# Kernel tuning notes

Measured on AMD Instinct MI355X. Metric: run time of the kernel, lower is better.

Reference implementation:

```python
import jax, jax.numpy as jnp
import numpy as np

B, S, TAGSET = 64, 512, 62
T = TAGSET + 2  # + START (index T-2) and END (index T-1)


def setup_inputs() -> dict:
    key = jax.random.key(0)
    k1, k2, k3, k4 = jax.random.split(key, 4)
    feats = jax.random.normal(k1, (B, S, T), dtype=jnp.float32)
    # transitions param (torch init is zeros; small random for a non-degenerate baseline)
    transitions = 0.01 * jax.random.normal(k2, (T, T), dtype=jnp.float32)
    # variable-length contiguous-prefix mask (CRF assumes mask[:, 0] == 1)
    lengths = jax.random.randint(k3, (B,), S // 2, S + 1)
    mask = (jnp.arange(S)[None, :] < lengths[:, None]).astype(jnp.int32)
    tags = jax.random.randint(k4, (B, S), 0, TAGSET).astype(jnp.int32)
    return {"feats": feats, "transitions": transitions, "mask": mask, "tags": tags}


def _nll(feats, transitions, mask, tags):
    b, s, t = feats.shape
    maskb = mask.astype(bool)
    feats_t = jnp.transpose(feats, (1, 0, 2))  # [S, B, T]
    mask_t = jnp.transpose(maskb, (1, 0))       # [S, B]

    # ---- partition function (calculate_PZ) ----
    start = t - 2
    init_part = feats_t[0] + transitions[start][None, :]  # [B, T]

    def step(part, inp):
        f_t, m_t = inp  # f_t: [B, T] emissions, m_t: [B]
        # scores[b, i, j] = part[b, i] + transitions[i, j] + f_t[b, j]
        cur = jax.nn.logsumexp(
            part[:, :, None] + transitions[None, :, :] + f_t[:, None, :], axis=1
        )  # [B, T]
        part = jnp.where(m_t[:, None], cur, part)
        return part, None

    part, _ = jax.lax.scan(step, init_part, (feats_t[1:], mask_t[1:]))
    final = jax.nn.logsumexp(part[:, :, None] + transitions[None, :, :], axis=1)
    forward_score = final[:, t - 1].sum()  # transition into END

    # ---- gold score (score_sentence) ----
    tags = tags.astype(jnp.int32)
    prev = jnp.concatenate(
        [jnp.full((b, 1), start, dtype=jnp.int32), tags[:, :-1]], axis=1
    )  # [B, S] previous tag (START at t=0)
    emit = jnp.take_along_axis(feats, tags[..., None].astype(jnp.int32), axis=2)[..., 0]
    trans = transitions[prev, tags]  # [B, S]
    tg_energy = jnp.where(maskb, emit + trans, 0.0).sum()
    lengths = mask.astype(jnp.int32).sum(axis=1)  # [B]
    end_ids = jnp.take_along_axis(tags, (lengths - 1)[:, None], axis=1)[:, 0]
    end_energy = transitions[end_ids, t - 1].sum()
    gold_score = tg_energy + end_energy

    return forward_score - gold_score


def reference(feats, transitions, mask, tags):
    return _nll(feats, transitions, mask, tags)
```

## Files before the change

kernel.cpp:

```cpp
#include <hip/hip_runtime.h>


#define SS 512
#define TT 64
#define CC 8
#define KCH 64
#define START_TAG 62
#define END_TAG 63
#define LOG2E_F 1.44269504088896340736f
#define LN2_F 0.69314718055994530942f

#define WS_ECOL_OFF 4194304
#define WS_GOLD_OFF 4325376
#define WS_EF_OFF   4325632
#define MSTR 72

typedef float v4f __attribute__((ext_vector_type(4)));
typedef _Float16 h4 __attribute__((ext_vector_type(4)));
typedef __fp16 c2 __attribute__((ext_vector_type(2)));
union H4u { h4 v; struct { c2 lo, hi; } p; };

__global__ __launch_bounds__(256, 1)
void crf_prep(const float* __restrict__ feats, const float* __restrict__ trans,
              const int* __restrict__ mask, const int* __restrict__ tags,
              float* __restrict__ out, float* __restrict__ Gg,
              _Float16* __restrict__ Ef) {
    const int c = blockIdx.x;
    const int tid = threadIdx.x;
    const int w = tid >> 6;
    __shared__ int li[4];
    __shared__ float gf[4];
    __shared__ int Lsh;

    int m = mask[c * SS + tid] + mask[c * SS + 256 + tid];
#pragma unroll
    for (int s_ = 1; s_ < 64; s_ <<= 1) m += __shfl_xor(m, s_, 64);
    if ((tid & 63) == 0) li[w] = m;
    __syncthreads();
    if (tid == 0) Lsh = li[0] + li[1] + li[2] + li[3];
    __syncthreads();
    const int Lc = Lsh;

    float g = 0.f;
#pragma unroll
    for (int rep = 0; rep < 2; ++rep) {
        int t = tid + rep * 256;
        if (t < Lc) {
            int cur = tags[c * SS + t];
            int prev = (t == 0) ? START_TAG : tags[c * SS + t - 1];
            g += feats[(size_t)c * SS * TT + (size_t)t * TT + cur] + trans[prev * TT + cur];
        }
    }
    if (tid == 0) g += trans[tags[c * SS + Lc - 1] * TT + END_TAG];
#pragma unroll
    for (int s_ = 1; s_ < 64; s_ <<= 1) g += __shfl_xor(g, s_, 64);
    if ((tid & 63) == 0) gf[w] = g;
    __syncthreads();
    if (tid == 0) Gg[c] = gf[0] + gf[1] + gf[2] + gf[3];

    if (c == 0) {
#pragma unroll
        for (int k = 0; k < 16; ++k) {
            int idx = tid + k * 256;
            Ef[idx] = (_Float16)expf(trans[idx]);
        }
        if (tid == 0) out[0] = 0.f;
    }
}

__device__ __forceinline__ void cstep(const h4 (&A)[4][4], h4 (&B)[4],
                                      float* __restrict__ emb, float& fq,
                                      const float* __restrict__ fcol, int tload,
                                      int q, int l, int& esum, int& esc) {
    v4f z = {0.f, 0.f, 0.f, 0.f};
    v4f D[4];
#pragma unroll
    for (int mt = 0; mt < 4; ++mt) {
        v4f a = __builtin_amdgcn_mfma_f32_16x16x16f16(A[mt][0], B[0], z, 0, 0, 0);
        a = __builtin_amdgcn_mfma_f32_16x16x16f16(A[mt][1], B[1], a, 0, 0, 0);
        v4f b = __builtin_amdgcn_mfma_f32_16x16x16f16(A[mt][2], B[2], z, 0, 0, 0);
        b = __builtin_amdgcn_mfma_f32_16x16x16f16(A[mt][3], B[3], b, 0, 0, 0);
        D[mt] = a + b;
    }
    v4f em[4];
#pragma unroll
    for (int mt = 0; mt < 4; ++mt) em[mt] = *(const v4f*)(emb + 16 * mt + 4 * q);
    emb[l] = __builtin_amdgcn_exp2f(fq * LOG2E_F);
    fq = fcol[(size_t)tload * TT];
    esum += esc;
    float scf = __uint_as_float((unsigned)(127 - esc) << 23);
    v4f qs[4];
#pragma unroll
    for (int mt = 0; mt < 4; ++mt) qs[mt] = D[mt] * (em[mt] * scf);
#pragma unroll
    for (int mt = 0; mt < 4; ++mt) {
        H4u u;
        u.p.lo = __builtin_amdgcn_cvt_pkrtz(qs[mt].x, qs[mt].y);
        u.p.hi = __builtin_amdgcn_cvt_pkrtz(qs[mt].z, qs[mt].w);
        B[mt] = u.v;
    }
    unsigned u0 = (unsigned)__builtin_amdgcn_readfirstlane((int)__float_as_uint(qs[0].x));
    esc = (int)((u0 >> 23) & 255u) - 127;
}

__global__ __launch_bounds__(256, 1)
void crf_chunks(const float* __restrict__ feats, const int* __restrict__ mask,
                const _Float16* __restrict__ Ef, unsigned short* __restrict__ Pg,
                int* __restrict__ Eg) {
    __shared__ float emA[4][2][TT];
    __shared__ float emB[4][2][TT];
    __shared__ __align__(16) _Float16 mld[TT * MSTR];
    __shared__ int ebuf[4];

    const int blk = blockIdx.x;
    const int chain = blk >> 3, c = blk & 7;
    const int tid = threadIdx.x;
    const int w = tid >> 6, l = tid & 63;
    const int n16 = l & 15, q = l >> 4;
    const int ncol = 16 * w + n16;

    h4 A[4][4];
#pragma unroll
    for (int mt = 0; mt < 4; ++mt)
#pragma unroll
        for (int ks = 0; ks < 4; ++ks) {
            h4 a;
#pragma unroll
            for (int e = 0; e < 4; ++e)
                a[e] = Ef[(16 * ks + 4 * q + e) * TT + 16 * mt + n16];
            A[mt][ks] = a;
        }

    const int* mp = mask + chain * SS;
    int msum = 0;
#pragma unroll
    for (int k = 0; k < 8; ++k) msum += mp[k * 64 + l];
#pragma unroll
    for (int s_ = 1; s_ < 64; s_ <<= 1) msum += __shfl_xor(msum, s_, 64);
    const int L = msum;

    const int t0a = 1 + KCH * c;
    const int t0b = t0a + 32;
    int nliveA = (L - 1) - KCH * c;
    nliveA = nliveA < 0 ? 0 : (nliveA > 32 ? 32 : nliveA);
    int nliveB = (L - 1) - KCH * c - 32;
    nliveB = nliveB < 0 ? 0 : (nliveB > 32 ? 32 : nliveB);

    h4 BA[4], BB[4];
#pragma unroll
    for (int ks = 0; ks < 4; ++ks) {
        h4 b;
#pragma unroll
        for (int j = 0; j < 4; ++j)
            b[j] = (_Float16)((16 * ks + 4 * q + j == ncol) ? 1.f : 0.f);
        BA[ks] = b;
        BB[ks] = b;
    }

    const float* fcol = feats + (size_t)chain * SS * TT + l;
#define CLAMP_T(x) ((x) < SS ? (x) : SS - 1)
    emA[w][0][l] = __builtin_amdgcn_exp2f(fcol[(size_t)CLAMP_T(t0a) * TT] * LOG2E_F);
    emA[w][1][l] = __builtin_amdgcn_exp2f(fcol[(size_t)CLAMP_T(t0a + 1) * TT] * LOG2E_F);
    emB[w][0][l] = __builtin_amdgcn_exp2f(fcol[(size_t)CLAMP_T(t0b) * TT] * LOG2E_F);
    emB[w][1][l] = __builtin_amdgcn_exp2f(fcol[(size_t)CLAMP_T(t0b + 1) * TT] * LOG2E_F);
    float fqA0 = fcol[(size_t)CLAMP_T(t0a + 2) * TT];
    float fqA1 = fcol[(size_t)CLAMP_T(t0a + 3) * TT];
    float fqB0 = fcol[(size_t)CLAMP_T(t0b + 2) * TT];
    float fqB1 = fcol[(size_t)CLAMP_T(t0b + 3) * TT];

    int esumA = 0, escA = 0, esumB = 0, escB = 0;

    const int nB2 = nliveB & ~1;
    int s = 0;
    for (; s < nB2; s += 2) {
        cstep(A, BA, &emA[w][0][0], fqA0, fcol, CLAMP_T(t0a + s + 4), q, l, esumA, escA);
        cstep(A, BB, &emB[w][0][0], fqB0, fcol, CLAMP_T(t0b + s + 4), q, l, esumB, escB);
        cstep(A, BA, &emA[w][1][0], fqA1, fcol, CLAMP_T(t0a + s + 5), q, l, esumA, escA);
        cstep(A, BB, &emB[w][1][0], fqB1, fcol, CLAMP_T(t0b + s + 5), q, l, esumB, escB);
    }
    if (nliveB & 1)
        cstep(A, BB, &emB[w][0][0], fqB0, fcol, SS - 1, q, l, esumB, escB);
    for (; s + 1 < nliveA; s += 2) {
        cstep(A, BA, &emA[w][0][0], fqA0, fcol, CLAMP_T(t0a + s + 4), q, l, esumA, escA);
        cstep(A, BA, &emA[w][1][0], fqA1, fcol, CLAMP_T(t0a + s + 5), q, l, esumA, escA);
    }
    if (s < nliveA)
        cstep(A, BA, &emA[w][0][0], fqA0, fcol, SS - 1, q, l, esumA, escA);
#undef CLAMP_T

    if (l == 0) ebuf[w] = esumB;
    __syncthreads();
    int eBmax = max(max(ebuf[0], ebuf[1]), max(ebuf[2], ebuf[3]));
    {
        _Float16 scl = (_Float16)ldexpf(1.f, esumB - eBmax);
        h4 s4 = {scl, scl, scl, scl};
#pragma unroll
        for (int ks = 0; ks < 4; ++ks) {
            h4 v = BB[ks] * s4;
#pragma unroll
            for (int j = 0; j < 4; ++j)
                mld[(16 * ks + 4 * q + j) * MSTR + ncol] = v[j];
        }
    }
    __syncthreads();
    h4 AH[4][4];
#pragma unroll
    for (int mt = 0; mt < 4; ++mt)
#pragma unroll
        for (int ks = 0; ks < 4; ++ks)
            AH[mt][ks] = *(const h4*)(mld + (16 * mt + n16) * MSTR + 16 * ks + 4 * q);
    v4f z = {0.f, 0.f, 0.f, 0.f};
    h4 Rf[4];
#pragma unroll
    for (int mt = 0; mt < 4; ++mt) {
        v4f a = __builtin_amdgcn_mfma_f32_16x16x16f16(AH[mt][0], BA[0], z, 0, 0, 0);
        a = __builtin_amdgcn_mfma_f32_16x16x16f16(AH[mt][1], BA[1], a, 0, 0, 0);
        v4f b = __builtin_amdgcn_mfma_f32_16x16x16f16(AH[mt][2], BA[2], z, 0, 0, 0);
        b = __builtin_amdgcn_mfma_f32_16x16x16f16(AH[mt][3], BA[3], b, 0, 0, 0);
        v4f d = a + b;
        H4u u;
        u.p.lo = __builtin_amdgcn_cvt_pkrtz(d.x, d.y);
        u.p.hi = __builtin_amdgcn_cvt_pkrtz(d.z, d.w);
        Rf[mt] = u.v;
    }
    __syncthreads();
#pragma unroll
    for (int mt = 0; mt < 4; ++mt)
#pragma unroll
        for (int j = 0; j < 4; ++j)
            mld[(16 * mt + 4 * q + j) * MSTR + ncol] = Rf[mt][j];
    __syncthreads();
    {
        const size_t base = ((size_t)chain * CC + c) * 4096;
        int r = tid >> 2, cb = tid & 3;
        const uint4* src = (const uint4*)(mld + r * MSTR + cb * 16);
        uint4* dst = (uint4*)(Pg + base + r * TT + cb * 16);
        dst[0] = src[0];
        dst[1] = src[1];
    }
    if (q == 0) Eg[(chain * CC + c) * TT + ncol] = esumA + eBmax;
}

__global__ __launch_bounds__(64, 1)
void crf_combine(const float* __restrict__ feats, const float* __restrict__ trans,
                 const unsigned short* __restrict__ Pg, const int* __restrict__ Eg,
                 const float* __restrict__ Gg, float* __restrict__ out) {
    __shared__ __align__(16) float yl[TT];
    const int chain = blockIdx.x;
    const int j = threadIdx.x;

    float part0 = feats[(size_t)chain * SS * TT + j] + trans[START_TAG * TT + j];
    float M0 = part0;
#pragma unroll
    for (int m = 1; m < 64; m <<= 1) M0 = fmaxf(M0, __shfl_xor(M0, m, 64));
    float x = exp2f((part0 - M0) * LOG2E_F);
    int esumX = 0;

    for (int c = 0; c < CC; ++c) {
        int e = Eg[(chain * CC + c) * TT + j];
        int emax = e;
#pragma unroll
        for (int m = 1; m < 64; m <<= 1) emax = max(emax, __shfl_xor(emax, m, 64));
        yl[j] = ldexpf(x, e - emax);
        float yv[64];
        {
            const uint4* yq = (const uint4*)yl;
#pragma unroll
            for (int i = 0; i < 16; ++i) {
                union { uint4 u; float f[4]; } cv;
                cv.u = yq[i];
                yv[4 * i + 0] = cv.f[0]; yv[4 * i + 1] = cv.f[1];
                yv[4 * i + 2] = cv.f[2]; yv[4 * i + 3] = cv.f[3];
            }
        }
        const uint4* rp = (const uint4*)(Pg + ((size_t)chain * CC + c) * 4096 + (size_t)j * TT);
        float acc = 0.f;
#pragma unroll
        for (int i = 0; i < 8; ++i) {
            union { uint4 u; _Float16 h[8]; } pv;
            pv.u = rp[i];
#pragma unroll
            for (int k2 = 0; k2 < 8; ++k2)
                acc = __builtin_fmaf((float)pv.h[k2], yv[8 * i + k2], acc);
        }
        float am = acc;
#pragma unroll
        for (int m = 1; m < 64; m <<= 1) am = fmaxf(am, __shfl_xor(am, m, 64));
        int e0 = (int)((__float_as_uint(am) >> 23) & 255u) - 127;
        x = ldexpf(acc, -e0);
        esumX += e0 + emax;
    }

    float val = x * expf(trans[j * TT + END_TAG]);
#pragma unroll
    for (int m = 1; m < 64; m <<= 1) val += __shfl_xor(val, m, 64);
    float fwd = logf(val) + (float)esumX * LN2_F + M0;
    if (j == 0) atomicAdd(out, fwd);

    if (chain == 0) {
        float gv = Gg[j];
#pragma unroll
        for (int m = 1; m < 64; m <<= 1) gv += __shfl_xor(gv, m, 64);
        if (j == 0) atomicAdd(out, -gv);
    }
}

extern "C" void kernel_launch(void* const* d_in, const int* in_sizes, int n_in,
                              void* d_out, int out_size, void* d_ws, size_t ws_size,
                              hipStream_t stream) {
    const float* feats = (const float*)d_in[0];
    const float* trans = (const float*)d_in[1];
    const int*   mask  = (const int*)d_in[2];
    const int*   tags  = (const int*)d_in[3];
    float* out = (float*)d_out;
    unsigned short* Pg = (unsigned short*)d_ws;
    int*       Eg = (int*)((char*)d_ws + WS_ECOL_OFF);
    float*     Gg = (float*)((char*)d_ws + WS_GOLD_OFF);
    _Float16*  Ef = (_Float16*)((char*)d_ws + WS_EF_OFF);

    crf_prep<<<dim3(64), dim3(256), 0, stream>>>(feats, trans, mask, tags, out, Gg, Ef);
    crf_chunks<<<dim3(64 * CC), dim3(256), 0, stream>>>(feats, mask, Ef, Pg, Eg);
    crf_combine<<<dim3(64), dim3(64), 0, stream>>>(feats, trans, Pg, Eg, Gg, out);
}
```

Measured before the change: 112.1 us.

## Fuse prep into chunk kernel, split chains into more chunks, prefetch in combine

Removes the separate prep kernel by folding the gold-score work into extra blocks of the chunk kernel, and computes exp(transitions) per block instead of reading a precomputed fp16 table. Each chain is split into 16 chunks when the workspace allows, giving more blocks and shorter sequential scans. Chunks now write both half-products separately instead of merging them with an in-block MFMA, so the combine kernel does twice as many sequential matvec steps; it prefetches the next product matrix to hide load latency. This trades shorter chunk critical paths and one fewer launch for a longer serial combine stage.

```diff
diff --git a/kernel.cpp b/kernel.cpp
--- a/kernel.cpp
+++ b/kernel.cpp
@@ -3,70 +3,16 @@
 
 #define SS 512
 #define TT 64
-#define CC 8
-#define KCH 64
 #define START_TAG 62
 #define END_TAG 63
 #define LOG2E_F 1.44269504088896340736f
 #define LN2_F 0.69314718055994530942f
-
-#define WS_ECOL_OFF 4194304
-#define WS_GOLD_OFF 4325376
-#define WS_EF_OFF   4325632
 #define MSTR 72
 
 typedef float v4f __attribute__((ext_vector_type(4)));
 typedef _Float16 h4 __attribute__((ext_vector_type(4)));
 typedef __fp16 c2 __attribute__((ext_vector_type(2)));
 union H4u { h4 v; struct { c2 lo, hi; } p; };
-
-__global__ __launch_bounds__(256, 1)
-void crf_prep(const float* __restrict__ feats, const float* __restrict__ trans,
-              const int* __restrict__ mask, const int* __restrict__ tags,
-              float* __restrict__ out, float* __restrict__ Gg,
-              _Float16* __restrict__ Ef) {
-    const int c = blockIdx.x;
-    const int tid = threadIdx.x;
-    const int w = tid >> 6;
-    __shared__ int li[4];
-    __shared__ float gf[4];
-    __shared__ int Lsh;
-
-    int m = mask[c * SS + tid] + mask[c * SS + 256 + tid];
-#pragma unroll
-    for (int s_ = 1; s_ < 64; s_ <<= 1) m += __shfl_xor(m, s_, 64);
-    if ((tid & 63) == 0) li[w] = m;
-    __syncthreads();
-    if (tid == 0) Lsh = li[0] + li[1] + li[2] + li[3];
-    __syncthreads();
-    const int Lc = Lsh;
-
-    float g = 0.f;
-#pragma unroll
-    for (int rep = 0; rep < 2; ++rep) {
-        int t = tid + rep * 256;
-        if (t < Lc) {
-            int cur = tags[c * SS + t];
-            int prev = (t == 0) ? START_TAG : tags[c * SS + t - 1];
-            g += feats[(size_t)c * SS * TT + (size_t)t * TT + cur] + trans[prev * TT + cur];
-        }
-    }
-    if (tid == 0) g += trans[tags[c * SS + Lc - 1] * TT + END_TAG];
-#pragma unroll
-    for (int s_ = 1; s_ < 64; s_ <<= 1) g += __shfl_xor(g, s_, 64);
-    if ((tid & 63) == 0) gf[w] = g;
-    __syncthreads();
-    if (tid == 0) Gg[c] = gf[0] + gf[1] + gf[2] + gf[3];
-
-    if (c == 0) {
-#pragma unroll
-        for (int k = 0; k < 16; ++k) {
-            int idx = tid + k * 256;
-            Ef[idx] = (_Float16)expf(trans[idx]);
-        }
-        if (tid == 0) out[0] = 0.f;
-    }
-}
 
 __device__ __forceinline__ void cstep(const h4 (&A)[4][4], h4 (&B)[4],
                                       float* __restrict__ emb, float& fq,
@@ -103,18 +49,60 @@
     esc = (int)((u0 >> 23) & 255u) - 127;
 }
 
+template <int CCT>
 __global__ __launch_bounds__(256, 1)
-void crf_chunks(const float* __restrict__ feats, const int* __restrict__ mask,
-                const _Float16* __restrict__ Ef, unsigned short* __restrict__ Pg,
-                int* __restrict__ Eg) {
-    __shared__ float emA[4][2][TT];
-    __shared__ float emB[4][2][TT];
+void crf_chunks(const float* __restrict__ feats, const float* __restrict__ trans,
+                const int* __restrict__ mask, const int* __restrict__ tags,
+                float* __restrict__ out, unsigned short* __restrict__ Pg,
+                int* __restrict__ Eg, float* __restrict__ Gg) {
+    constexpr int KCH_T = SS / CCT;
+    constexpr int HALF = KCH_T / 2;
+    constexpr int M = 2 * CCT;
+
+    __shared__ __align__(16) float emA[4][2][TT];
+    __shared__ __align__(16) float emB[4][2][TT];
     __shared__ __align__(16) _Float16 mld[TT * MSTR];
-    __shared__ int ebuf[4];
+    __shared__ int li[4];
+    __shared__ float gf[4];
+    __shared__ int Lsh;
 
     const int blk = blockIdx.x;
-    const int chain = blk >> 3, c = blk & 7;
     const int tid = threadIdx.x;
+
+    if (blk >= 64 * CCT) {
+        const int chain = blk - 64 * CCT;
+        const int w = tid >> 6;
+        int m = mask[chain * SS + tid] + mask[chain * SS + 256 + tid];
+#pragma unroll
+        for (int s_ = 1; s_ < 64; s_ <<= 1) m += __shfl_xor(m, s_, 64);
+        if ((tid & 63) == 0) li[w] = m;
+        __syncthreads();
+        if (tid == 0) Lsh = li[0] + li[1] + li[2] + li[3];
+        __syncthreads();
+        const int Lc = Lsh;
+
+        float g = 0.f;
+#pragma unroll
+        for (int rep = 0; rep < 2; ++rep) {
+            int t = tid + rep * 256;
+            if (t < Lc) {
+                int cur = tags[chain * SS + t];
+                int prev = (t == 0) ? START_TAG : tags[chain * SS + t - 1];
+                g += feats[(size_t)chain * SS * TT + (size_t)t * TT + cur]
+                   + trans[prev * TT + cur];
+            }
+        }
+        if (tid == 0) g += trans[tags[chain * SS + Lc - 1] * TT + END_TAG];
+#pragma unroll
+        for (int s_ = 1; s_ < 64; s_ <<= 1) g += __shfl_xor(g, s_, 64);
+        if ((tid & 63) == 0) gf[w] = g;
+        __syncthreads();
+        if (tid == 0) Gg[chain] = gf[0] + gf[1] + gf[2] + gf[3];
+        if (chain == 0 && tid == 0) out[0] = 0.f;
+        return;
+    }
+
+    const int chain = blk / CCT, c = blk % CCT;
     const int w = tid >> 6, l = tid & 63;
     const int n16 = l & 15, q = l >> 4;
     const int ncol = 16 * w + n16;
@@ -127,7 +115,7 @@
             h4 a;
 #pragma unroll
             for (int e = 0; e < 4; ++e)
-                a[e] = Ef[(16 * ks + 4 * q + e) * TT + 16 * mt + n16];
+                a[e] = (_Float16)expf(trans[(16 * ks + 4 * q + e) * TT + 16 * mt + n16]);
             A[mt][ks] = a;
         }
 
@@ -139,12 +127,12 @@
     for (int s_ = 1; s_ < 64; s_ <<= 1) msum += __shfl_xor(msum, s_, 64);
     const int L = msum;
 
-    const int t0a = 1 + KCH * c;
-    const int t0b = t0a + 32;
-    int nliveA = (L - 1) - KCH * c;
-    nliveA = nliveA < 0 ? 0 : (nliveA > 32 ? 32 : nliveA);
-    int nliveB = (L - 1) - KCH * c - 32;
-    nliveB = nliveB < 0 ? 0 : (nliveB > 32 ? 32 : nliveB);
+    const int t0a = 1 + KCH_T * c;
+    const int t0b = t0a + HALF;
+    int nliveA = (L - 1) - KCH_T * c;
+    nliveA = nliveA < 0 ? 0 : (nliveA > HALF ? HALF : nliveA);
+    int nliveB = (L - 1) - KCH_T * c - HALF;
+    nliveB = nliveB < 0 ? 0 : (nliveB > HALF ? HALF : nliveB);
 
     h4 BA[4], BB[4];
 #pragma unroll
@@ -188,63 +176,44 @@
         cstep(A, BA, &emA[w][0][0], fqA0, fcol, SS - 1, q, l, esumA, escA);
 #undef CLAMP_T
 
-    if (l == 0) ebuf[w] = esumB;
-    __syncthreads();
-    int eBmax = max(max(ebuf[0], ebuf[1]), max(ebuf[2], ebuf[3]));
-    {
-        _Float16 scl = (_Float16)ldexpf(1.f, esumB - eBmax);
-        h4 s4 = {scl, scl, scl, scl};
-#pragma unroll
-        for (int ks = 0; ks < 4; ++ks) {
-            h4 v = BB[ks] * s4;
-#pragma unroll
-            for (int j = 0; j < 4; ++j)
-                mld[(16 * ks + 4 * q + j) * MSTR + ncol] = v[j];
-        }
-    }
-    __syncthreads();
-    h4 AH[4][4];
-#pragma unroll
-    for (int mt = 0; mt < 4; ++mt)
-#pragma unroll
-        for (int ks = 0; ks < 4; ++ks)
-            AH[mt][ks] = *(const h4*)(mld + (16 * mt + n16) * MSTR + 16 * ks + 4 * q);
-    v4f z = {0.f, 0.f, 0.f, 0.f};
-    h4 Rf[4];
-#pragma unroll
-    for (int mt = 0; mt < 4; ++mt) {
-        v4f a = __builtin_amdgcn_mfma_f32_16x16x16f16(AH[mt][0], BA[0], z, 0, 0, 0);
-        a = __builtin_amdgcn_mfma_f32_16x16x16f16(AH[mt][1], BA[1], a, 0, 0, 0);
-        v4f b = __builtin_amdgcn_mfma_f32_16x16x16f16(AH[mt][2], BA[2], z, 0, 0, 0);
-        b = __builtin_amdgcn_mfma_f32_16x16x16f16(AH[mt][3], BA[3], b, 0, 0, 0);
-        v4f d = a + b;
-        H4u u;
-        u.p.lo = __builtin_amdgcn_cvt_pkrtz(d.x, d.y);
-        u.p.hi = __builtin_amdgcn_cvt_pkrtz(d.z, d.w);
-        Rf[mt] = u.v;
-    }
-    __syncthreads();
-#pragma unroll
-    for (int mt = 0; mt < 4; ++mt)
+    const size_t pbase = ((size_t)chain * M + 2 * c) * 4096;
+#pragma unroll
+    for (int ks = 0; ks < 4; ++ks)
 #pragma unroll
         for (int j = 0; j < 4; ++j)
-            mld[(16 * mt + 4 * q + j) * MSTR + ncol] = Rf[mt][j];
+            mld[(16 * ks + 4 * q + j) * MSTR + ncol] = BA[ks][j];
     __syncthreads();
     {
-        const size_t base = ((size_t)chain * CC + c) * 4096;
         int r = tid >> 2, cb = tid & 3;
         const uint4* src = (const uint4*)(mld + r * MSTR + cb * 16);
-        uint4* dst = (uint4*)(Pg + base + r * TT + cb * 16);
+        uint4* dst = (uint4*)(Pg + pbase + r * TT + cb * 16);
         dst[0] = src[0];
         dst[1] = src[1];
     }
-    if (q == 0) Eg[(chain * CC + c) * TT + ncol] = esumA + eBmax;
+    if (q == 0) Eg[(chain * M + 2 * c) * TT + ncol] = esumA;
+    __syncthreads();
+#pragma unroll
+    for (int ks = 0; ks < 4; ++ks)
+#pragma unroll
+        for (int j = 0; j < 4; ++j)
+            mld[(16 * ks + 4 * q + j) * MSTR + ncol] = BB[ks][j];
+    __syncthreads();
+    {
+        int r = tid >> 2, cb = tid & 3;
+        const uint4* src = (const uint4*)(mld + r * MSTR + cb * 16);
+        uint4* dst = (uint4*)(Pg + pbase + 4096 + r * TT + cb * 16);
+        dst[0] = src[0];
+        dst[1] = src[1];
+    }
+    if (q == 0) Eg[(chain * M + 2 * c + 1) * TT + ncol] = esumB;
 }
 
+template <int CCT>
 __global__ __launch_bounds__(64, 1)
 void crf_combine(const float* __restrict__ feats, const float* __restrict__ trans,
                  const unsigned short* __restrict__ Pg, const int* __restrict__ Eg,
                  const float* __restrict__ Gg, float* __restrict__ out) {
+    constexpr int M = 2 * CCT;
     __shared__ __align__(16) float yl[TT];
     const int chain = blockIdx.x;
     const int j = threadIdx.x;
@@ -256,12 +225,30 @@
     float x = exp2f((part0 - M0) * LOG2E_F);
     int esumX = 0;
 
-    for (int c = 0; c < CC; ++c) {
-        int e = Eg[(chain * CC + c) * TT + j];
-        int emax = e;
+    uint4 rbuf[8];
+    {
+        const uint4* rp = (const uint4*)(Pg + ((size_t)chain * M) * 4096 + (size_t)j * TT);
+#pragma unroll
+        for (int i = 0; i < 8; ++i) rbuf[i] = rp[i];
+    }
+    int epre = Eg[(chain * M) * TT + j];
+
+    for (int mm = 0; mm < M; ++mm) {
+        int ecur = epre;
+        uint4 rcur[8];
+#pragma unroll
+        for (int i = 0; i < 8; ++i) rcur[i] = rbuf[i];
+        if (mm + 1 < M) {
+            const uint4* rn = (const uint4*)(Pg + ((size_t)chain * M + mm + 1) * 4096 + (size_t)j * TT);
+#pragma unroll
+            for (int i = 0; i < 8; ++i) rbuf[i] = rn[i];
+            epre = Eg[(chain * M + mm + 1) * TT + j];
+        }
+
+        int emax = ecur;
 #pragma unroll
         for (int m = 1; m < 64; m <<= 1) emax = max(emax, __shfl_xor(emax, m, 64));
-        yl[j] = ldexpf(x, e - emax);
+        yl[j] = ldexpf(x, ecur - emax);
         float yv[64];
         {
             const uint4* yq = (const uint4*)yl;
@@ -273,12 +260,11 @@
                 yv[4 * i + 2] = cv.f[2]; yv[4 * i + 3] = cv.f[3];
             }
         }
-        const uint4* rp = (const uint4*)(Pg + ((size_t)chain * CC + c) * 4096 + (size_t)j * TT);
         float acc = 0.f;
 #pragma unroll
         for (int i = 0; i < 8; ++i) {
             union { uint4 u; _Float16 h[8]; } pv;
-            pv.u = rp[i];
+            pv.u = rcur[i];
 #pragma unroll
             for (int k2 = 0; k2 < 8; ++k2)
                 acc = __builtin_fmaf((float)pv.h[k2], yv[8 * i + k2], acc);
@@ -313,12 +299,26 @@
     const int*   mask  = (const int*)d_in[2];
     const int*   tags  = (const int*)d_in[3];
     float* out = (float*)d_out;
-    unsigned short* Pg = (unsigned short*)d_ws;
-    int*       Eg = (int*)((char*)d_ws + WS_ECOL_OFF);
-    float*     Gg = (float*)((char*)d_ws + WS_GOLD_OFF);
-    _Float16*  Ef = (_Float16*)((char*)d_ws + WS_EF_OFF);
-
-    crf_prep<<<dim3(64), dim3(256), 0, stream>>>(feats, trans, mask, tags, out, Gg, Ef);
-    crf_chunks<<<dim3(64 * CC), dim3(256), 0, stream>>>(feats, mask, Ef, Pg, Eg);
-    crf_combine<<<dim3(64), dim3(64), 0, stream>>>(feats, trans, Pg, Eg, Gg, out);
+
+    const size_t pb16 = 64ull * 32 * 8192, eb16 = 64ull * 32 * 256;
+    const size_t need16 = pb16 + eb16 + 256;
+
+    if (ws_size >= need16) {
+        constexpr int C = 16;
+        unsigned short* Pg = (unsigned short*)d_ws;
+        int*   Eg = (int*)((char*)d_ws + pb16);
+        float* Gg = (float*)((char*)d_ws + pb16 + eb16);
+        crf_chunks<C><<<dim3(64 * C + 64), dim3(256), 0, stream>>>(feats, trans, mask, tags,
+                                                                   out, Pg, Eg, Gg);
+        crf_combine<C><<<dim3(64), dim3(64), 0, stream>>>(feats, trans, Pg, Eg, Gg, out);
+    } else {
+        constexpr int C = 8;
+        const size_t pb8 = 64ull * 16 * 8192, eb8 = 64ull * 16 * 256;
+        unsigned short* Pg = (unsigned short*)d_ws;
+        int*   Eg = (int*)((char*)d_ws + pb8);
+        float* Gg = (float*)((char*)d_ws + pb8 + eb8);
+        crf_chunks<C><<<dim3(64 * C + 64), dim3(256), 0, stream>>>(feats, trans, mask, tags,
+                                                                   out, Pg, Eg, Gg);
+        crf_combine<C><<<dim3(64), dim3(64), 0, stream>>>(feats, trans, Pg, Eg, Gg, out);
+    }
 }
```

New measurement: 135.0 us. +20.5%, slower.
